# Kernel optimization log

Measured on AMD Instinct MI355X. Metric: run time of the kernel, lower is better.

Reference implementation:

```python
import jax, jax.numpy as jnp
import numpy as np

C_ATOM = 128
N_HEADS = 4
HEAD_DIM = C_ATOM // N_HEADS


def setup_inputs() -> dict:
    key = jax.random.key(0)
    ks = jax.random.split(key, 11)
    B, L, A = 16, 4096, 4
    x = jax.random.normal(ks[0], (B, L, A, C_ATOM), dtype=jnp.float32)
    mask = jax.random.randint(ks[1], (B, L, A), 0, 2) > 0
    mask = mask.at[..., 0].set(True)  # ensure >=1 valid atom per residue (avoids all--inf softmax)
    s = 1.0 / np.sqrt(C_ATOM)
    def lin(k):
        kw, kb = jax.random.split(k)
        W = jax.random.uniform(kw, (C_ATOM, C_ATOM), jnp.float32, -s, s)
        b = jax.random.uniform(kb, (C_ATOM,), jnp.float32, -s, s)
        return W, b
    Wq, bq = lin(ks[2])
    Wk, bk = lin(ks[3])
    Wv, bv = lin(ks[4])
    Wo, bo = lin(ks[5])
    return {"x": x, "mask": mask, "Wq": Wq, "bq": bq, "Wk": Wk, "bk": bk,
            "Wv": Wv, "bv": bv, "Wo": Wo, "bo": bo}


def reference(x, mask, Wq, bq, Wk, bk, Wv, bv, Wo, bo):
    B, L, A, C = x.shape
    H, D = N_HEADS, HEAD_DIM
    # q/k/v projections (torch Linear: x @ W.T + b)
    q = (x @ Wq.T + bq).reshape(B, L, A, H, D)
    k = (x @ Wk.T + bk).reshape(B, L, A, H, D)
    v = (x @ Wv.T + bv).reshape(B, L, A, H, D)
    scale = 1.0 / jnp.sqrt(jnp.asarray(D, x.dtype))
    # per-residue 4x4 attention scores: [B, L, H, q_atom, k_atom]
    scores = jnp.einsum("blqhd,blkhd->blhqk", q, k) * scale
    # key-side mask bias (broadcast over heads and query atoms)
    bias = jnp.where(mask[:, :, None, None, :], 0.0, -jnp.inf).astype(x.dtype)
    attn = jax.nn.softmax(scores + bias, axis=-1)
    out = jnp.einsum("blhqk,blkhd->blqhd", attn, v).reshape(B, L, A, C)
    out = out @ Wo.T + bo
    residue_mask = jnp.any(mask, axis=-1)[..., None, None].astype(out.dtype)  # [B,L,1,1]
    return out * residue_mask
```

## Files before the change

### kernel.cpp

```cpp
#include <hip/hip_runtime.h>
#include <stdint.h>


typedef __fp16 f16;
typedef f16   f16x2 __attribute__((ext_vector_type(2)));
typedef f16   f16x4 __attribute__((ext_vector_type(4)));
typedef f16   f16x8 __attribute__((ext_vector_type(8)));
typedef float f32x4 __attribute__((ext_vector_type(4)));

#define N_RES 65536
#define RPB   16
#define MROWS 64
#define CDIM  128
#define XSP   132
#define SOP   136

__device__ __forceinline__ uint32_t pkh(float a, float b) {
    f16x2 h = __builtin_amdgcn_cvt_pkrtz(a, b);
    return __builtin_bit_cast(uint32_t, h);
}

__global__ void wconv_kernel(const float* __restrict__ wq, const float* __restrict__ wk,
                             const float* __restrict__ wv, const float* __restrict__ wo,
                             uint16_t* __restrict__ dst) {
    int i = blockIdx.x * 256 + threadIdx.x;
    const float* s = (i < 16384) ? wq : (i < 32768) ? wk : (i < 49152) ? wv : wo;
    f16 h = (f16)s[i & 16383];
    dst[i] = __builtin_bit_cast(uint16_t, h);
}

template <bool USEWS>
__device__ __forceinline__ f16x8 ldw16(const uint16_t* __restrict__ wbf,
                                       const float* __restrict__ w32,
                                       int goff, int row, int col) {
    if constexpr (USEWS) {
        return *(const f16x8*)(wbf + goff + row * CDIM + col);
    } else {
        const float4* p = (const float4*)(w32 + row * CDIM + col);
        float4 a = p[0], b = p[1];
        uint4 u = make_uint4(pkh(a.x, a.y), pkh(a.z, a.w), pkh(b.x, b.y), pkh(b.z, b.w));
        return __builtin_bit_cast(f16x8, u);
    }
}

template <bool USEWS>
__global__ __launch_bounds__(256, 3)
void laa_main(const float* __restrict__ x, const int* __restrict__ mask,
              const float* __restrict__ Wq, const float* __restrict__ bq,
              const float* __restrict__ Wk, const float* __restrict__ bk,
              const float* __restrict__ Wv, const float* __restrict__ bv,
              const float* __restrict__ Wo, const float* __restrict__ bo,
              const uint16_t* __restrict__ wbf,
              float* __restrict__ out) {
    __shared__ float smem[MROWS * XSP];
    float*    xs = smem;
    uint16_t* sO = (uint16_t*)smem;
    float*    os = smem;

    const int tid  = threadIdx.x;
    const int wave = tid >> 6;
    const int lane = tid & 63;
    const int l15  = lane & 15;
    const int quad = lane >> 4;
    const int hb   = wave * 32;
    const long m0  = (long)blockIdx.x * MROWS;

    const f32x4 vzero = {0.f, 0.f, 0.f, 0.f};

    int4 mk4[4];
    #pragma unroll
    for (int m = 0; m < 4; ++m)
        mk4[m] = *(const int4*)(mask + ((long)blockIdx.x * RPB + m * 4 + quad) * 4);

    const float s = 0.17677669529663689f;
    float bqs[8], bks[8];
    #pragma unroll
    for (int nd = 0; nd < 2; ++nd) {
        float4 q4 = *(const float4*)(bq + hb + nd * 16 + quad * 4);
        float4 k4 = *(const float4*)(bk + hb + nd * 16 + quad * 4);
        bqs[nd * 4 + 0] = q4.x * s; bqs[nd * 4 + 1] = q4.y * s;
        bqs[nd * 4 + 2] = q4.z * s; bqs[nd * 4 + 3] = q4.w * s;
        bks[nd * 4 + 0] = k4.x;     bks[nd * 4 + 1] = k4.y;
        bks[nd * 4 + 2] = k4.z;     bks[nd * 4 + 3] = k4.w;
    }
    const float bvv0 = bv[hb + l15],      bvv1 = bv[hb + 16 + l15];
    const float bo0  = bo[hb + l15],      bo1  = bo[hb + 16 + l15];

    {
        const float4* xg = (const float4*)(x + m0 * CDIM);
        float4 xr[8];
        #pragma unroll
        for (int j = 0; j < 8; ++j) xr[j] = xg[tid + 256 * j];
        #pragma unroll
        for (int j = 0; j < 8; ++j) {
            int gi = tid + 256 * j;
            int r = gi >> 5, c = gi & 31;
            *(float4*)(xs + r * XSP + c * 4) = xr[j];
        }
    }
    __syncthreads();

    f32x4 qt[4][2], kt[4][2], vv[4][2];
    #pragma unroll
    for (int m = 0; m < 4; ++m)
        #pragma unroll
        for (int n = 0; n < 2; ++n) { qt[m][n] = vzero; kt[m][n] = vzero; vv[m][n] = vzero; }

    #pragma unroll
    for (int ks = 0; ks < 4; ++ks) {
        f16x8 xf[4];
        #pragma unroll
        for (int m = 0; m < 4; ++m) {
            const float* rp = xs + (m * 16 + l15) * XSP + ks * 32 + quad * 8;
            float4 a = *(const float4*)rp;
            float4 b = *(const float4*)(rp + 4);
            uint4 u = make_uint4(pkh(a.x, a.y), pkh(a.z, a.w), pkh(b.x, b.y), pkh(b.z, b.w));
            xf[m] = __builtin_bit_cast(f16x8, u);
        }
        f16x8 wqf[2], wkf[2], wvf[2];
        #pragma unroll
        for (int nt = 0; nt < 2; ++nt) {
            int row = hb + nt * 16 + l15, col = ks * 32 + quad * 8;
            wqf[nt] = ldw16<USEWS>(wbf, Wq, 0,     row, col);
            wkf[nt] = ldw16<USEWS>(wbf, Wk, 16384, row, col);
            wvf[nt] = ldw16<USEWS>(wbf, Wv, 32768, row, col);
        }
        #pragma unroll
        for (int m = 0; m < 4; ++m) {
            #pragma unroll
            for (int nt = 0; nt < 2; ++nt) {
                qt[m][nt] = __builtin_amdgcn_mfma_f32_16x16x32_f16(wqf[nt], xf[m], qt[m][nt], 0, 0, 0);
                kt[m][nt] = __builtin_amdgcn_mfma_f32_16x16x32_f16(wkf[nt], xf[m], kt[m][nt], 0, 0, 0);
                vv[m][nt] = __builtin_amdgcn_mfma_f32_16x16x32_f16(xf[m], wvf[nt], vv[m][nt], 0, 0, 0);
            }
        }
    }

    __syncthreads();

    float rm[4];
    const bool diag = (quad == (l15 >> 2));
    #pragma unroll
    for (int m = 0; m < 4; ++m) {
        uint4 uq, uk;
        uq.x = pkh(qt[m][0][0] * s + bqs[0], qt[m][0][1] * s + bqs[1]);
        uq.y = pkh(qt[m][0][2] * s + bqs[2], qt[m][0][3] * s + bqs[3]);
        uq.z = pkh(qt[m][1][0] * s + bqs[4], qt[m][1][1] * s + bqs[5]);
        uq.w = pkh(qt[m][1][2] * s + bqs[6], qt[m][1][3] * s + bqs[7]);
        uk.x = pkh(kt[m][0][0] + bks[0], kt[m][0][1] + bks[1]);
        uk.y = pkh(kt[m][0][2] + bks[2], kt[m][0][3] + bks[3]);
        uk.z = pkh(kt[m][1][0] + bks[4], kt[m][1][1] + bks[5]);
        uk.w = pkh(kt[m][1][2] + bks[6], kt[m][1][3] + bks[7]);
        f16x8 qtf = __builtin_bit_cast(f16x8, uq);
        f16x8 ktf = __builtin_bit_cast(f16x8, uk);
        f32x4 st = __builtin_amdgcn_mfma_f32_16x16x32_f16(ktf, qtf, vzero, 0, 0, 0);

        const int4 mk = mk4[m];
        rm[m] = (mk.x | mk.y | mk.z | mk.w) ? 1.f : 0.f;
        float mx = -3e38f;
        if (mk.x) mx = fmaxf(mx, st[0]);
        if (mk.y) mx = fmaxf(mx, st[1]);
        if (mk.z) mx = fmaxf(mx, st[2]);
        if (mk.w) mx = fmaxf(mx, st[3]);
        float e0 = mk.x ? __expf(st[0] - mx) : 0.f;
        float e1 = mk.y ? __expf(st[1] - mx) : 0.f;
        float e2 = mk.z ? __expf(st[2] - mx) : 0.f;
        float e3 = mk.w ? __expf(st[3] - mx) : 0.f;
        float inv = 1.f / (e0 + e1 + e2 + e3);
        uint2 up = make_uint2(diag ? pkh(e0 * inv, e1 * inv) : 0u,
                              diag ? pkh(e2 * inv, e3 * inv) : 0u);
        f16x4 pf = __builtin_bit_cast(f16x4, up);

        #pragma unroll
        for (int nt = 0; nt < 2; ++nt) {
            float bb = nt ? bvv1 : bvv0;
            uint2 uv = make_uint2(pkh(vv[m][nt][0] + bb, vv[m][nt][1] + bb),
                                  pkh(vv[m][nt][2] + bb, vv[m][nt][3] + bb));
            f16x4 vbf = __builtin_bit_cast(f16x4, uv);
            f32x4 ot = __builtin_amdgcn_mfma_f32_16x16x16f16(vbf, pf, vzero, 0, 0, 0);
            uint2 w2 = make_uint2(pkh(ot[0], ot[1]), pkh(ot[2], ot[3]));
            *(uint2*)(sO + (m * 16 + l15) * SOP + hb + nt * 16 + quad * 4) = w2;
        }
    }
    __syncthreads();

    f32x4 acc2[4][2];
    #pragma unroll
    for (int m = 0; m < 4; ++m)
        #pragma unroll
        for (int nt = 0; nt < 2; ++nt) acc2[m][nt] = vzero;

    #pragma unroll
    for (int ks = 0; ks < 4; ++ks) {
        f16x8 a2[4];
        #pragma unroll
        for (int m = 0; m < 4; ++m)
            a2[m] = *(const f16x8*)(sO + (m * 16 + l15) * SOP + ks * 32 + quad * 8);
        f16x8 b2[2];
        #pragma unroll
        for (int nt = 0; nt < 2; ++nt)
            b2[nt] = ldw16<USEWS>(wbf, Wo, 49152, hb + nt * 16 + l15, ks * 32 + quad * 8);
        #pragma unroll
        for (int m = 0; m < 4; ++m)
            #pragma unroll
            for (int nt = 0; nt < 2; ++nt)
                acc2[m][nt] = __builtin_amdgcn_mfma_f32_16x16x32_f16(a2[m], b2[nt], acc2[m][nt], 0, 0, 0);
    }

    __syncthreads();

    {
        #pragma unroll
        for (int m = 0; m < 4; ++m) {
            #pragma unroll
            for (int nt = 0; nt < 2; ++nt) {
                float bb = nt ? bo1 : bo0;
                #pragma unroll
                for (int r = 0; r < 4; ++r)
                    os[(m * 16 + quad * 4 + r) * XSP + hb + nt * 16 + l15] =
                        (acc2[m][nt][r] + bb) * rm[m];
            }
        }
    }
    __syncthreads();

    {
        float4* og = (float4*)(out + m0 * CDIM);
        #pragma unroll
        for (int j = 0; j < 8; ++j) {
            int gi = tid + 256 * j;
            int r = gi >> 5, c = gi & 31;
            *(og + gi) = *(const float4*)(os + r * XSP + c * 4);
        }
    }
}

extern "C" void kernel_launch(void* const* d_in, const int* in_sizes, int n_in,
                              void* d_out, int out_size, void* d_ws, size_t ws_size,
                              hipStream_t stream) {
    const float* x    = (const float*)d_in[0];
    const int*   mask = (const int*)d_in[1];
    const float* Wq   = (const float*)d_in[2];
    const float* bq   = (const float*)d_in[3];
    const float* Wk   = (const float*)d_in[4];
    const float* bk   = (const float*)d_in[5];
    const float* Wv   = (const float*)d_in[6];
    const float* bv   = (const float*)d_in[7];
    const float* Wo   = (const float*)d_in[8];
    const float* bo   = (const float*)d_in[9];
    float* out = (float*)d_out;

    const int nblocks = N_RES / RPB;
    const bool usews = ws_size >= (size_t)(4 * 16384 * sizeof(uint16_t));
    if (usews) {
        uint16_t* wbf = (uint16_t*)d_ws;
        wconv_kernel<<<256, 256, 0, stream>>>(Wq, Wk, Wv, Wo, wbf);
        laa_main<true><<<nblocks, 256, 0, stream>>>(x, mask, Wq, bq, Wk, bk, Wv, bv,
                                                    Wo, bo, wbf, out);
    } else {
        laa_main<false><<<nblocks, 256, 0, stream>>>(x, mask, Wq, bq, Wk, bk, Wv, bv,
                                                     Wo, bo, nullptr, out);
    }
}
```

Before: 328.2 us.

## Prefetch fp16 weights into registers up front and lower occupancy target

Loads all Q/K/V weight fragments into registers at kernel start, together with the x tile, so global weight latency overlaps the x load rather than sitting inside the MFMA loop. The output-projection weights are likewise fetched right after the QKV GEMM, before the attention step. Launch bounds drop from 3 to 2 blocks per CU to make room for the many extra live registers. This trades occupancy and register pressure for earlier, better-overlapped memory traffic.

```diff
diff --git a/kernel.cpp b/kernel.cpp
--- a/kernel.cpp
+++ b/kernel.cpp
@@ -29,22 +29,15 @@
     dst[i] = __builtin_bit_cast(uint16_t, h);
 }
 
+__device__ __forceinline__ f16x8 ldw32(const float* __restrict__ w32, int row, int col) {
+    const float4* p = (const float4*)(w32 + row * CDIM + col);
+    float4 a = p[0], b = p[1];
+    uint4 u = make_uint4(pkh(a.x, a.y), pkh(a.z, a.w), pkh(b.x, b.y), pkh(b.z, b.w));
+    return __builtin_bit_cast(f16x8, u);
+}
+
 template <bool USEWS>
-__device__ __forceinline__ f16x8 ldw16(const uint16_t* __restrict__ wbf,
-                                       const float* __restrict__ w32,
-                                       int goff, int row, int col) {
-    if constexpr (USEWS) {
-        return *(const f16x8*)(wbf + goff + row * CDIM + col);
-    } else {
-        const float4* p = (const float4*)(w32 + row * CDIM + col);
-        float4 a = p[0], b = p[1];
-        uint4 u = make_uint4(pkh(a.x, a.y), pkh(a.z, a.w), pkh(b.x, b.y), pkh(b.z, b.w));
-        return __builtin_bit_cast(f16x8, u);
-    }
-}
-
-template <bool USEWS>
-__global__ __launch_bounds__(256, 3)
+__global__ __launch_bounds__(256, 2)
 void laa_main(const float* __restrict__ x, const int* __restrict__ mask,
               const float* __restrict__ Wq, const float* __restrict__ bq,
               const float* __restrict__ Wk, const float* __restrict__ bk,
@@ -67,6 +60,24 @@
 
     const f32x4 vzero = {0.f, 0.f, 0.f, 0.f};
 
+    f16x8 wqr[4][2], wkr[4][2], wvr[4][2];
+    if constexpr (USEWS) {
+        #pragma unroll
+        for (int ks = 0; ks < 4; ++ks)
+            #pragma unroll
+            for (int nt = 0; nt < 2; ++nt) {
+                int off = (hb + nt * 16 + l15) * CDIM + ks * 32 + quad * 8;
+                wqr[ks][nt] = *(const f16x8*)(wbf + off);
+                wkr[ks][nt] = *(const f16x8*)(wbf + 16384 + off);
+                wvr[ks][nt] = *(const f16x8*)(wbf + 32768 + off);
+            }
+    }
+    float4 xr[8];
+    {
+        const float4* xg = (const float4*)(x + m0 * CDIM);
+        #pragma unroll
+        for (int j = 0; j < 8; ++j) xr[j] = xg[tid + 256 * j];
+    }
     int4 mk4[4];
     #pragma unroll
     for (int m = 0; m < 4; ++m)
@@ -86,17 +97,11 @@
     const float bvv0 = bv[hb + l15],      bvv1 = bv[hb + 16 + l15];
     const float bo0  = bo[hb + l15],      bo1  = bo[hb + 16 + l15];
 
-    {
-        const float4* xg = (const float4*)(x + m0 * CDIM);
-        float4 xr[8];
-        #pragma unroll
-        for (int j = 0; j < 8; ++j) xr[j] = xg[tid + 256 * j];
-        #pragma unroll
-        for (int j = 0; j < 8; ++j) {
-            int gi = tid + 256 * j;
-            int r = gi >> 5, c = gi & 31;
-            *(float4*)(xs + r * XSP + c * 4) = xr[j];
-        }
+    #pragma unroll
+    for (int j = 0; j < 8; ++j) {
+        int gi = tid + 256 * j;
+        int r = gi >> 5, c = gi & 31;
+        *(float4*)(xs + r * XSP + c * 4) = xr[j];
     }
     __syncthreads();
 
@@ -120,10 +125,14 @@
         f16x8 wqf[2], wkf[2], wvf[2];
         #pragma unroll
         for (int nt = 0; nt < 2; ++nt) {
-            int row = hb + nt * 16 + l15, col = ks * 32 + quad * 8;
-            wqf[nt] = ldw16<USEWS>(wbf, Wq, 0,     row, col);
-            wkf[nt] = ldw16<USEWS>(wbf, Wk, 16384, row, col);
-            wvf[nt] = ldw16<USEWS>(wbf, Wv, 32768, row, col);
+            if constexpr (USEWS) {
+                wqf[nt] = wqr[ks][nt]; wkf[nt] = wkr[ks][nt]; wvf[nt] = wvr[ks][nt];
+            } else {
+                int row = hb + nt * 16 + l15, col = ks * 32 + quad * 8;
+                wqf[nt] = ldw32(Wq, row, col);
+                wkf[nt] = ldw32(Wk, row, col);
+                wvf[nt] = ldw32(Wv, row, col);
+            }
         }
         #pragma unroll
         for (int m = 0; m < 4; ++m) {
@@ -137,6 +146,16 @@
     }
 
     __syncthreads();
+
+    f16x8 wor[4][2];
+    if constexpr (USEWS) {
+        #pragma unroll
+        for (int ks = 0; ks < 4; ++ks)
+            #pragma unroll
+            for (int nt = 0; nt < 2; ++nt)
+                wor[ks][nt] = *(const f16x8*)(wbf + 49152 +
+                    (hb + nt * 16 + l15) * CDIM + ks * 32 + quad * 8);
+    }
 
     float rm[4];
     const bool diag = (quad == (l15 >> 2));
@@ -198,8 +217,13 @@
             a2[m] = *(const f16x8*)(sO + (m * 16 + l15) * SOP + ks * 32 + quad * 8);
         f16x8 b2[2];
         #pragma unroll
-        for (int nt = 0; nt < 2; ++nt)
-            b2[nt] = ldw16<USEWS>(wbf, Wo, 49152, hb + nt * 16 + l15, ks * 32 + quad * 8);
+        for (int nt = 0; nt < 2; ++nt) {
+            if constexpr (USEWS) {
+                b2[nt] = wor[ks][nt];
+            } else {
+                b2[nt] = ldw32(Wo, hb + nt * 16 + l15, ks * 32 + quad * 8);
+            }
+        }
         #pragma unroll
         for (int m = 0; m < 4; ++m)
             #pragma unroll
```

Result: faster. 279.7 us (-14.8%).
